# Kernel tuning notes

Hardware: AMD Instinct MI355X
Metric: run time of the kernel (lower is better)

## Reference

```python
import jax, jax.numpy as jnp
import numpy as np

B, T = 4096, 2048
VOCAB, E, H = 1000, 8, 8


def setup_inputs() -> dict:
    key = jax.random.key(0)
    ks = jax.random.split(key, 8)
    x = jax.random.randint(ks[0], (B, T), 0, VOCAB)
    emb = jax.random.normal(ks[1], (VOCAB, E), dtype=jnp.float32)
    s = 1.0 / np.sqrt(H)
    W_ih = jax.random.uniform(ks[2], (4 * H, E), minval=-s, maxval=s, dtype=jnp.float32)
    W_hh = jax.random.uniform(ks[3], (4 * H, H), minval=-s, maxval=s, dtype=jnp.float32)
    b_ih = jax.random.uniform(ks[4], (4 * H,), minval=-s, maxval=s, dtype=jnp.float32)
    b_hh = jax.random.uniform(ks[5], (4 * H,), minval=-s, maxval=s, dtype=jnp.float32)
    W_cls = jax.random.uniform(ks[6], (1, H), minval=-s, maxval=s, dtype=jnp.float32)
    b_cls = jax.random.uniform(ks[7], (1,), minval=-s, maxval=s, dtype=jnp.float32)
    return {"x": x, "emb": emb, "W_ih": W_ih, "W_hh": W_hh, "b_ih": b_ih,
            "b_hh": b_hh, "W_cls": W_cls, "b_cls": b_cls}


def reference(x, emb, W_ih, W_hh, b_ih, b_hh, W_cls, b_cls):
    embeds = emb[x]  # [B, T, E]
    # Precompute input contribution to all 4 gates (i, f, g, o order like PyTorch).
    xg = jnp.einsum('bte,ge->btg', embeds, W_ih) + (b_ih + b_hh)  # [B, T, 4H]

    def step(carry, xg_t):
        h, c = carry
        gates = xg_t + h @ W_hh.T  # [B, 4H]
        i, f, g, o = jnp.split(gates, 4, axis=-1)
        i = jax.nn.sigmoid(i)
        f = jax.nn.sigmoid(f)
        g = jnp.tanh(g)
        o = jax.nn.sigmoid(o)
        c = f * c + i * g
        h = o * jnp.tanh(c)
        return (h, c), None

    h0 = jnp.zeros((x.shape[0], W_hh.shape[1]), dtype=emb.dtype)
    (h_last, _), _ = jax.lax.scan(step, (h0, h0), jnp.swapaxes(xg, 0, 1))
    out = jax.nn.sigmoid(h_last @ W_cls.T + b_cls)  # [B, 1]
    return out
```

## Files before the change

### kernel.cpp

```cpp
#include <hip/hip_runtime.h>

#define TT 2048
#define NV 1000
#define LOG2E 1.4426950408889634f

typedef float f32x2 __attribute__((ext_vector_type(2)));

__device__ __forceinline__ float tanh_fast(float x) {
    const float L = 7.90531110763549805f;
    x = __builtin_amdgcn_fmed3f(x, -L, L);
    float x2 = x * x;
    float p = -2.76076847742355e-16f;
    p = __builtin_fmaf(p, x2, 2.00018790482477e-13f);
    p = __builtin_fmaf(p, x2, -8.60467152213735e-11f);
    p = __builtin_fmaf(p, x2, 5.12229709037114e-08f);
    p = __builtin_fmaf(p, x2, 1.48572235717979e-05f);
    p = __builtin_fmaf(p, x2, 6.37261928875436e-04f);
    p = __builtin_fmaf(p, x2, 4.89352455891786e-03f);
    float q = 1.19825839466702e-06f;
    q = __builtin_fmaf(q, x2, 1.18534705686654e-04f);
    q = __builtin_fmaf(q, x2, 2.26843463243900e-03f);
    q = __builtin_fmaf(q, x2, 4.89352518554385e-03f);
    float r = __builtin_amdgcn_rcpf(q);
    return (x * p) * r;
}

template <int CTRL>
__device__ __forceinline__ float dppf(float x) {
    return __int_as_float(__builtin_amdgcn_update_dpp(
        0, __float_as_int(x), CTRL, 0xF, 0xF, true));
}
#define DPP_XOR1 0xB1
#define DPP_XOR2 0x4E
#define DPP_XOR3 0x1B
#define DPP_ROR4 0x124
#define DPP_HMIR 0x141
#define DPP_ROR8 0x128

__device__ __forceinline__ f32x2 pkfma(f32x2 a, float b, f32x2 c) {
    return __builtin_elementwise_fma(a, (f32x2){b, b}, c);
}

extern "C" __global__ void __launch_bounds__(256, 1)
lstm_fused(const int* __restrict__ x, const float* __restrict__ emb,
           const float* __restrict__ W_ih, const float* __restrict__ W_hh,
           const float* __restrict__ b_ih, const float* __restrict__ b_hh,
           const float* __restrict__ W_cls, const float* __restrict__ b_cls,
           float* __restrict__ out)
{
    extern __shared__ float TAB[];

    const int tid = threadIdx.x;
    const int l   = tid & 15;
    const int s   = l >> 3;
    const int j   = l & 7;
    const int grp = tid >> 4;

    const int glo = j + (s << 4);
    const int ghi = glo + 8;
    const float scx = s ? (-2.0f * LOG2E) : -LOG2E;
    const float scy = -LOG2E;
    const float Ax = s ? (-4.0f * LOG2E) : 1.0f;
    const float Bx = s ? ( 2.0f * LOG2E) : 0.0f;
    const bool is0 = (s == 0);

    {
        float wl[8], wh[8];
        #pragma unroll
        for (int k = 0; k < 8; ++k) {
            wl[k] = W_ih[glo * 8 + k];
            wh[k] = W_ih[ghi * 8 + k];
        }
        const float bl = b_ih[glo] + b_hh[glo];
        const float bh = b_ih[ghi] + b_hh[ghi];
        for (int v = grp; v < NV; v += 16) {
            const float4 e0 = *(const float4*)(emb + v * 8);
            const float4 e1 = *(const float4*)(emb + v * 8 + 4);
            float dl = bl + e0.x*wl[0] + e0.y*wl[1] + e0.z*wl[2] + e0.w*wl[3]
                          + e1.x*wl[4] + e1.y*wl[5] + e1.z*wl[6] + e1.w*wl[7];
            float dh = bh + e0.x*wh[0] + e0.y*wh[1] + e0.z*wh[2] + e0.w*wh[3]
                          + e1.x*wh[4] + e1.y*wh[5] + e1.z*wh[6] + e1.w*wh[7];
            *(float2*)(TAB + v * 32 + l * 2) = make_float2(scx * dl, scy * dh);
        }
    }
    __syncthreads();

    const int b = blockIdx.x * 16 + grp;
    const int* __restrict__ xrow = x + (size_t)b * TT;
    const char* __restrict__ TABl = (const char*)TAB + l * 8;

    f32x2 wpk[8];
    #pragma unroll
    for (int m = 0; m < 8; ++m) {
        wpk[m].x = scx * W_hh[glo * 8 + (j ^ m)];
        wpk[m].y = scy * W_hh[ghi * 8 + (j ^ m)];
    }

    float cs = 0.0f;
    float hn = 0.0f;

    int4 iA = *(const int4*)(xrow);
    int4 iB = *(const int4*)(xrow + 4);
    f32x2 xg0 = *(const f32x2*)(TABl + (iA.x << 7));
    f32x2 xg1 = *(const f32x2*)(TABl + (iA.y << 7));

#define STEP(XG, NIDX) do {                                                      \
        float mm  = dppf<DPP_HMIR>(hn);                       \
        f32x2 uA = pkfma(wpk[0], hn, XG);                                        \
        f32x2 uB = wpk[1] * (f32x2){dppf<DPP_XOR1>(hn), dppf<DPP_XOR1>(hn)};     \
        uA = pkfma(wpk[2], dppf<DPP_XOR2>(hn), uA);                              \
        uB = pkfma(wpk[3], dppf<DPP_XOR3>(hn), uB);                              \
        uA = pkfma(wpk[4], dppf<DPP_XOR3>(mm), uA);                              \
        uB = pkfma(wpk[5], dppf<DPP_XOR2>(mm), uB);                              \
        uA = pkfma(wpk[6], dppf<DPP_XOR1>(mm), uA);                              \
        uB = pkfma(wpk[7], mm, uB);                                              \
        f32x2 u = uA + uB;           \
        XG = *(const f32x2*)(TABl + ((NIDX) << 7));            \
        float el = __builtin_amdgcn_exp2f(u.x);                                  \
        float ey = __builtin_amdgcn_exp2f(u.y);                                  \
        float r  = __builtin_amdgcn_rcpf(1.0f + el);                             \
        float aLk = __builtin_fmaf(Ax, r, Bx);           \
        float sy = __builtin_amdgcn_rcpf(1.0f + ey);          \
        float IG  = dppf<DPP_ROR8>(aLk) * aLk;       \
        float pHi = dppf<DPP_ROR8>(sy);                                          \
        float F   = is0 ? sy : pHi;                                  \
        float O   = is0 ? pHi : sy;                                  \
        float twoO = O + O;                                                      \
        cs = __builtin_fmaf(F, cs, IG);                            \
        float ec = __builtin_amdgcn_exp2f(cs);            \
        float rc = __builtin_amdgcn_rcpf(1.0f + ec);                             \
        hn = __builtin_fmaf(twoO, rc, -O);                      \
    } while (0)

    for (int t = 0; t < TT; t += 4) {
        const int nb = (t + 8 < TT) ? (t / 4 + 2) : 0;
        int4 iN = *(const int4*)(xrow + nb * 4);
        STEP(xg0, iA.z);
        STEP(xg1, iA.w);
        STEP(xg0, iB.x);
        STEP(xg1, iB.y);
        iA = iB; iB = iN;
    }
#undef STEP

    {
        float v1 = dppf<DPP_XOR1>(hn);
        float v2 = dppf<DPP_XOR2>(hn);
        float v3 = dppf<DPP_XOR3>(hn);
        float v4 = dppf<DPP_ROR4>(hn);
        float v5 = dppf<DPP_XOR1>(v4);
        float v6 = dppf<DPP_XOR2>(v4);
        float v7 = dppf<DPP_XOR3>(v4);
        if (l == 0) {
            float z = b_cls[0]
                + hn * W_cls[0] + v1 * W_cls[1] + v2 * W_cls[2] + v3 * W_cls[3]
                + v4 * W_cls[4] + v5 * W_cls[5] + v6 * W_cls[6] + v7 * W_cls[7];
            out[b] = __builtin_fmaf(0.5f, tanh_fast(0.5f * z), 0.5f);
        }
    }
}

extern "C" void kernel_launch(void* const* d_in, const int* in_sizes, int n_in,
                              void* d_out, int out_size, void* d_ws, size_t ws_size,
                              hipStream_t stream)
{
    (void)in_sizes; (void)n_in; (void)d_ws; (void)ws_size; (void)out_size;
    const int*   x     = (const int*)  d_in[0];
    const float* emb   = (const float*)d_in[1];
    const float* W_ih  = (const float*)d_in[2];
    const float* W_hh  = (const float*)d_in[3];
    const float* b_ih  = (const float*)d_in[4];
    const float* b_hh  = (const float*)d_in[5];
    const float* W_cls = (const float*)d_in[6];
    const float* b_cls = (const float*)d_in[7];
    float* out = (float*)d_out;

    const int lds_bytes = NV * 16 * 8;
    hipFuncSetAttribute((const void*)lstm_fused,
                        hipFuncAttributeMaxDynamicSharedMemorySize, lds_bytes);

    lstm_fused<<<dim3(256), dim3(256), lds_bytes, stream>>>(
        x, emb, W_ih, W_hh, b_ih, b_hh, W_cls, b_cls, out);
}
```

Measured before the change: 274.7 us.

## Interleave two independent LSTM batch rows per thread group for ILP

Each 16-lane group now advances two independent sequences at once, interleaving their recurrent step instructions so one chain's latency hides behind the other's. The grid is halved to 128 blocks to match. This trades parallelism across CUs for instruction-level parallelism: only 128 of the MI355X's CUs are used and register pressure rises, while the serial dependency chain per step is now shared between two rows.

```diff
diff --git a/kernel.cpp b/kernel.cpp
--- a/kernel.cpp
+++ b/kernel.cpp
@@ -85,8 +85,10 @@
     }
     __syncthreads();
 
-    const int b = blockIdx.x * 16 + grp;
-    const int* __restrict__ xrow = x + (size_t)b * TT;
+    const int bA = blockIdx.x * 32 + grp;
+    const int bB = bA + 16;
+    const int* __restrict__ xrowA = x + (size_t)bA * TT;
+    const int* __restrict__ xrowB = x + (size_t)bB * TT;
     const char* __restrict__ TABl = (const char*)TAB + l * 8;
 
     f32x2 wpk[8];
@@ -96,66 +98,110 @@
         wpk[m].y = scy * W_hh[ghi * 8 + (j ^ m)];
     }
 
-    float cs = 0.0f;
-    float hn = 0.0f;
-
-    int4 iA = *(const int4*)(xrow);
-    int4 iB = *(const int4*)(xrow + 4);
-    f32x2 xg0 = *(const f32x2*)(TABl + (iA.x << 7));
-    f32x2 xg1 = *(const f32x2*)(TABl + (iA.y << 7));
-
-#define STEP(XG, NIDX) do {                                                      \
-        float mm  = dppf<DPP_HMIR>(hn);                       \
-        f32x2 uA = pkfma(wpk[0], hn, XG);                                        \
-        f32x2 uB = wpk[1] * (f32x2){dppf<DPP_XOR1>(hn), dppf<DPP_XOR1>(hn)};     \
-        uA = pkfma(wpk[2], dppf<DPP_XOR2>(hn), uA);                              \
-        uB = pkfma(wpk[3], dppf<DPP_XOR3>(hn), uB);                              \
-        uA = pkfma(wpk[4], dppf<DPP_XOR3>(mm), uA);                              \
-        uB = pkfma(wpk[5], dppf<DPP_XOR2>(mm), uB);                              \
-        uA = pkfma(wpk[6], dppf<DPP_XOR1>(mm), uA);                              \
-        uB = pkfma(wpk[7], mm, uB);                                              \
-        f32x2 u = uA + uB;           \
-        XG = *(const f32x2*)(TABl + ((NIDX) << 7));            \
-        float el = __builtin_amdgcn_exp2f(u.x);                                  \
-        float ey = __builtin_amdgcn_exp2f(u.y);                                  \
-        float r  = __builtin_amdgcn_rcpf(1.0f + el);                             \
-        float aLk = __builtin_fmaf(Ax, r, Bx);           \
-        float sy = __builtin_amdgcn_rcpf(1.0f + ey);          \
-        float IG  = dppf<DPP_ROR8>(aLk) * aLk;       \
-        float pHi = dppf<DPP_ROR8>(sy);                                          \
-        float F   = is0 ? sy : pHi;                                  \
-        float O   = is0 ? pHi : sy;                                  \
-        float twoO = O + O;                                                      \
-        cs = __builtin_fmaf(F, cs, IG);                            \
-        float ec = __builtin_amdgcn_exp2f(cs);            \
-        float rc = __builtin_amdgcn_rcpf(1.0f + ec);                             \
-        hn = __builtin_fmaf(twoO, rc, -O);                      \
+    float csA = 0.0f, hnA = 0.0f;
+    float csB = 0.0f, hnB = 0.0f;
+
+    int4 iAa = *(const int4*)(xrowA);
+    int4 iBa = *(const int4*)(xrowA + 4);
+    int4 iAb = *(const int4*)(xrowB);
+    int4 iBb = *(const int4*)(xrowB + 4);
+    f32x2 xg0a = *(const f32x2*)(TABl + (iAa.x << 7));
+    f32x2 xg1a = *(const f32x2*)(TABl + (iAa.y << 7));
+    f32x2 xg0b = *(const f32x2*)(TABl + (iAb.x << 7));
+    f32x2 xg1b = *(const f32x2*)(TABl + (iAb.y << 7));
+
+#define STEP_AB(XGa, XGb, NIa, NIb) do {                                         \
+        float mmA = dppf<DPP_HMIR>(hnA);                                         \
+        float mmB = dppf<DPP_HMIR>(hnB);                                         \
+        f32x2 uAa = pkfma(wpk[0], hnA, XGa);                                     \
+        f32x2 uAb = pkfma(wpk[0], hnB, XGb);                                     \
+        float h1a = dppf<DPP_XOR1>(hnA);                                         \
+        float h1b = dppf<DPP_XOR1>(hnB);                                         \
+        f32x2 uBa = wpk[1] * (f32x2){h1a, h1a};                                  \
+        f32x2 uBb = wpk[1] * (f32x2){h1b, h1b};                                  \
+        uAa = pkfma(wpk[2], dppf<DPP_XOR2>(hnA), uAa);                           \
+        uAb = pkfma(wpk[2], dppf<DPP_XOR2>(hnB), uAb);                           \
+        uBa = pkfma(wpk[3], dppf<DPP_XOR3>(hnA), uBa);                           \
+        uBb = pkfma(wpk[3], dppf<DPP_XOR3>(hnB), uBb);                           \
+        uAa = pkfma(wpk[4], dppf<DPP_XOR3>(mmA), uAa);                           \
+        uAb = pkfma(wpk[4], dppf<DPP_XOR3>(mmB), uAb);                           \
+        uBa = pkfma(wpk[5], dppf<DPP_XOR2>(mmA), uBa);                           \
+        uBb = pkfma(wpk[5], dppf<DPP_XOR2>(mmB), uBb);                           \
+        uAa = pkfma(wpk[6], dppf<DPP_XOR1>(mmA), uAa);                           \
+        uAb = pkfma(wpk[6], dppf<DPP_XOR1>(mmB), uAb);                           \
+        uBa = pkfma(wpk[7], mmA, uBa);                                           \
+        uBb = pkfma(wpk[7], mmB, uBb);                                           \
+        f32x2 ua = uAa + uBa;                                                    \
+        f32x2 ub = uAb + uBb;                                                    \
+        XGa = *(const f32x2*)(TABl + ((NIa) << 7));            \
+        XGb = *(const f32x2*)(TABl + ((NIb) << 7));                              \
+        float elA = __builtin_amdgcn_exp2f(ua.x);                                \
+        float elB = __builtin_amdgcn_exp2f(ub.x);                                \
+        float eyA = __builtin_amdgcn_exp2f(ua.y);                                \
+        float eyB = __builtin_amdgcn_exp2f(ub.y);                                \
+        float rA  = __builtin_amdgcn_rcpf(1.0f + elA);                           \
+        float rB  = __builtin_amdgcn_rcpf(1.0f + elB);                           \
+        float aLkA = __builtin_fmaf(Ax, rA, Bx);                                 \
+        float aLkB = __builtin_fmaf(Ax, rB, Bx);                                 \
+        float syA = __builtin_amdgcn_rcpf(1.0f + eyA);                           \
+        float syB = __builtin_amdgcn_rcpf(1.0f + eyB);                           \
+        float IGA = dppf<DPP_ROR8>(aLkA) * aLkA;                                 \
+        float IGB = dppf<DPP_ROR8>(aLkB) * aLkB;                                 \
+        float pHiA = dppf<DPP_ROR8>(syA);                                        \
+        float pHiB = dppf<DPP_ROR8>(syB);                                        \
+        float FA = is0 ? syA : pHiA;                                             \
+        float FB = is0 ? syB : pHiB;                                             \
+        float OA = is0 ? pHiA : syA;                                             \
+        float OB = is0 ? pHiB : syB;                                             \
+        float twoOA = OA + OA;                                                   \
+        float twoOB = OB + OB;                                                   \
+        csA = __builtin_fmaf(FA, csA, IGA);                                      \
+        csB = __builtin_fmaf(FB, csB, IGB);                                      \
+        float ecA = __builtin_amdgcn_exp2f(csA);                                 \
+        float ecB = __builtin_amdgcn_exp2f(csB);                                 \
+        float rcA = __builtin_amdgcn_rcpf(1.0f + ecA);                           \
+        float rcB = __builtin_amdgcn_rcpf(1.0f + ecB);                           \
+        hnA = __builtin_fmaf(twoOA, rcA, -OA);                                   \
+        hnB = __builtin_fmaf(twoOB, rcB, -OB);                                   \
     } while (0)
 
     for (int t = 0; t < TT; t += 4) {
         const int nb = (t + 8 < TT) ? (t / 4 + 2) : 0;
-        int4 iN = *(const int4*)(xrow + nb * 4);
-        STEP(xg0, iA.z);
-        STEP(xg1, iA.w);
-        STEP(xg0, iB.x);
-        STEP(xg1, iB.y);
-        iA = iB; iB = iN;
-    }
-#undef STEP
+        int4 iNa = *(const int4*)(xrowA + nb * 4);
+        int4 iNb = *(const int4*)(xrowB + nb * 4);
+        STEP_AB(xg0a, xg0b, iAa.z, iAb.z);
+        STEP_AB(xg1a, xg1b, iAa.w, iAb.w);
+        STEP_AB(xg0a, xg0b, iBa.x, iBb.x);
+        STEP_AB(xg1a, xg1b, iBa.y, iBb.y);
+        iAa = iBa; iBa = iNa;
+        iAb = iBb; iBb = iNb;
+    }
+#undef STEP_AB
 
     {
-        float v1 = dppf<DPP_XOR1>(hn);
-        float v2 = dppf<DPP_XOR2>(hn);
-        float v3 = dppf<DPP_XOR3>(hn);
-        float v4 = dppf<DPP_ROR4>(hn);
+        float v1 = dppf<DPP_XOR1>(hnA);
+        float v2 = dppf<DPP_XOR2>(hnA);
+        float v3 = dppf<DPP_XOR3>(hnA);
+        float v4 = dppf<DPP_ROR4>(hnA);
         float v5 = dppf<DPP_XOR1>(v4);
         float v6 = dppf<DPP_XOR2>(v4);
         float v7 = dppf<DPP_XOR3>(v4);
+        float w1 = dppf<DPP_XOR1>(hnB);
+        float w2 = dppf<DPP_XOR2>(hnB);
+        float w3 = dppf<DPP_XOR3>(hnB);
+        float w4 = dppf<DPP_ROR4>(hnB);
+        float w5 = dppf<DPP_XOR1>(w4);
+        float w6 = dppf<DPP_XOR2>(w4);
+        float w7 = dppf<DPP_XOR3>(w4);
         if (l == 0) {
-            float z = b_cls[0]
-                + hn * W_cls[0] + v1 * W_cls[1] + v2 * W_cls[2] + v3 * W_cls[3]
+            float zA = b_cls[0]
+                + hnA * W_cls[0] + v1 * W_cls[1] + v2 * W_cls[2] + v3 * W_cls[3]
                 + v4 * W_cls[4] + v5 * W_cls[5] + v6 * W_cls[6] + v7 * W_cls[7];
-            out[b] = __builtin_fmaf(0.5f, tanh_fast(0.5f * z), 0.5f);
+            out[bA] = __builtin_fmaf(0.5f, tanh_fast(0.5f * zA), 0.5f);
+            float zB = b_cls[0]
+                + hnB * W_cls[0] + w1 * W_cls[1] + w2 * W_cls[2] + w3 * W_cls[3]
+                + w4 * W_cls[4] + w5 * W_cls[5] + w6 * W_cls[6] + w7 * W_cls[7];
+            out[bB] = __builtin_fmaf(0.5f, tanh_fast(0.5f * zB), 0.5f);
         }
     }
 }
@@ -179,6 +225,6 @@
     hipFuncSetAttribute((const void*)lstm_fused,
                         hipFuncAttributeMaxDynamicSharedMemorySize, lds_bytes);
 
-    lstm_fused<<<dim3(256), dim3(256), lds_bytes, stream>>>(
+    lstm_fused<<<dim3(128), dim3(256), lds_bytes, stream>>>(
         x, emb, W_ih, W_hh, b_ih, b_hh, W_cls, b_cls, out);
 }
```

Result: slower. 426.6 us (+55.3%).
